# Kernel optimization log

Measured on AMD Instinct MI355X. Metric: run time of the kernel, lower is better.

## Reference

```python
import jax, jax.numpy as jnp
import numpy as np

N = 100000      # n_entities + n_users (graph nodes)
E = 1600000     # edges
R = 8           # relations
D = 64          # entity_dim
DR = 64         # relation_dim
EPS = 1e-12


def setup_inputs() -> dict:
    key = jax.random.key(0)
    ks = jax.random.split(key, 16)
    inp = {
        'entity_emb': jax.random.normal(ks[0], (N, D), jnp.float32) * 0.1,
        'rel_emb':    jax.random.normal(ks[1], (R, DR), jnp.float32) * 0.1,
        'W_R':        jax.random.normal(ks[2], (R, D, DR), jnp.float32) * 0.1,
        'W1_0': jax.random.normal(ks[3], (32, 64), jnp.float32) * 0.1,
        'b1_0': jax.random.normal(ks[4], (32,), jnp.float32) * 0.1,
        'W2_0': jax.random.normal(ks[5], (32, 64), jnp.float32) * 0.1,
        'b2_0': jax.random.normal(ks[6], (32,), jnp.float32) * 0.1,
        'W1_1': jax.random.normal(ks[7], (16, 32), jnp.float32) * 0.1,
        'b1_1': jax.random.normal(ks[8], (16,), jnp.float32) * 0.1,
        'W2_1': jax.random.normal(ks[9], (16, 32), jnp.float32) * 0.1,
        'b2_1': jax.random.normal(ks[10], (16,), jnp.float32) * 0.1,
        'src':   jax.random.randint(ks[11], (E,), 0, N, dtype=jnp.int32),
        'dst':   jax.random.randint(ks[12], (E,), 0, N, dtype=jnp.int32),
        'etype': jax.random.randint(ks[13], (E,), 0, R, dtype=jnp.int32),
    }
    return inp


def _l2_normalize(x):
    # F.normalize(x, p=2, dim=1)
    n = jnp.linalg.norm(x, axis=1, keepdims=True)
    return x / jnp.maximum(n, EPS)


def reference(entity_emb, rel_emb, W_R, W1_0, b1_0, W2_0, b2_0,
              W1_1, b1_1, W2_1, b2_1, src, dst, etype):
    # ---- compute_attention: per-edge relation-specific projection ----
    # proj[n, r, :] = entity_emb[n] @ W_R[r]   -> [N, R, DR]
    proj = jnp.einsum('nd,rdk->nrk', entity_emb, W_R)
    r_mul_t = proj[src, etype]          # [E, DR] (edges.src)
    r_mul_h = proj[dst, etype]          # [E, DR] (edges.dst)
    r_e = rel_emb[etype]                # [E, DR]
    att = jnp.sum(r_mul_t * jnp.tanh(r_mul_h + r_e), axis=-1)  # [E]

    # ---- edge_softmax: normalize over incoming edges of each dst ----
    m = jax.ops.segment_max(att, dst, num_segments=N)           # [N]
    ex = jnp.exp(att - m[dst])
    s = jax.ops.segment_sum(ex, dst, num_segments=N)            # [N]
    a = ex / s[dst]                                             # [E]

    # ---- bi-interaction aggregator layers ----
    def agg_layer(x, W1, b1, W2, b2):
        msg = x[src] * a[:, None]                               # u_mul_e
        Nh = jax.ops.segment_sum(msg, dst, num_segments=N)      # sum to dst
        out1 = jax.nn.leaky_relu(jnp.matmul(x + Nh, W1.T) + b1, 0.01)
        out2 = jax.nn.leaky_relu(jnp.matmul(x * Nh, W2.T) + b2, 0.01)
        return _l2_normalize(out1 + out2)

    ego = entity_emb
    h1 = agg_layer(ego, W1_0, b1_0, W2_0, b2_0)   # [N, 32]
    h2 = agg_layer(h1, W1_1, b1_1, W2_1, b2_1)    # [N, 16]
    all_embed = jnp.concatenate([ego, h1, h2], axis=1)  # [N, 112]
    return all_embed
```

## Files before the change

kernel.cpp:

```cpp
#include <hip/hip_runtime.h>
#include <hip/hip_bf16.h>
#include <math.h>

#define NN 100000
#define NE 1600000
#define NR 8
#define DD 64
#define DDR 64

typedef __attribute__((ext_vector_type(8))) short bf8v;
typedef __attribute__((ext_vector_type(4))) float f4v;

__device__ __forceinline__ unsigned enc_f(float f) {
    unsigned u = __float_as_uint(f);
    return (u & 0x80000000u) ? ~u : (u | 0x80000000u);
}
__device__ __forceinline__ float dec_f(unsigned u) {
    return (u & 0x80000000u) ? __uint_as_float(u & 0x7FFFFFFFu) : __uint_as_float(~u);
}

__device__ __forceinline__ float bflo(unsigned u) { return __uint_as_float(u << 16); }
__device__ __forceinline__ float bfhi(unsigned u) { return __uint_as_float(u & 0xFFFF0000u); }
__device__ __forceinline__ short f2bfs(float x) {
    __hip_bfloat16 h = __float2bfloat16(x);
    return *reinterpret_cast<short*>(&h);
}

__device__ __forceinline__ float tanh_fast(float x) {
    x = fminf(fmaxf(x, -15.f), 15.f);
    float e = __expf(2.f * x);
    return (e - 1.f) * __builtin_amdgcn_rcpf(e + 1.f);
}

__global__ void __launch_bounds__(256)
k_projm(const float* __restrict__ emb, const float* __restrict__ WR,
        unsigned short* __restrict__ proj)
{
    int t = threadIdx.x;
    int wv = t >> 6, l = t & 63;
    int lo = l & 15, hi = l >> 4;
    int r = blockIdx.y;
    int colbase = (wv & 1) * 32;
    int nwbase = blockIdx.x * 128 + (wv >> 1) * 64;

    const float* __restrict__ wb = WR + (long)r * (DD * DDR) + (hi * 8) * DDR + colbase + lo;
    bf8v B00, B01, B10, B11;
#pragma unroll
    for (int j = 0; j < 8; ++j) {
        B00[j] = f2bfs(wb[(0 * 32 + j) * DDR + 0]);
        B01[j] = f2bfs(wb[(1 * 32 + j) * DDR + 0]);
        B10[j] = f2bfs(wb[(0 * 32 + j) * DDR + 16]);
        B11[j] = f2bfs(wb[(1 * 32 + j) * DDR + 16]);
    }

    for (int nt = 0; nt < 4; ++nt) {
        int nb = nwbase + nt * 16;
        int arow = nb + lo;
        float4 xa0 = make_float4(0.f, 0.f, 0.f, 0.f), xa1 = xa0, xb0 = xa0, xb1 = xa0;
        if (arow < NN) {
            const float* __restrict__ xr = emb + (long)arow * DD + hi * 8;
            xa0 = *(const float4*)(xr);
            xa1 = *(const float4*)(xr + 4);
            xb0 = *(const float4*)(xr + 32);
            xb1 = *(const float4*)(xr + 36);
        }
        bf8v A0, A1;
        A0[0] = f2bfs(xa0.x); A0[1] = f2bfs(xa0.y); A0[2] = f2bfs(xa0.z); A0[3] = f2bfs(xa0.w);
        A0[4] = f2bfs(xa1.x); A0[5] = f2bfs(xa1.y); A0[6] = f2bfs(xa1.z); A0[7] = f2bfs(xa1.w);
        A1[0] = f2bfs(xb0.x); A1[1] = f2bfs(xb0.y); A1[2] = f2bfs(xb0.z); A1[3] = f2bfs(xb0.w);
        A1[4] = f2bfs(xb1.x); A1[5] = f2bfs(xb1.y); A1[6] = f2bfs(xb1.z); A1[7] = f2bfs(xb1.w);

        f4v acc0 = {0.f, 0.f, 0.f, 0.f}, acc1 = {0.f, 0.f, 0.f, 0.f};
        acc0 = __builtin_amdgcn_mfma_f32_16x16x32_bf16(A0, B00, acc0, 0, 0, 0);
        acc0 = __builtin_amdgcn_mfma_f32_16x16x32_bf16(A1, B01, acc0, 0, 0, 0);
        acc1 = __builtin_amdgcn_mfma_f32_16x16x32_bf16(A0, B10, acc1, 0, 0, 0);
        acc1 = __builtin_amdgcn_mfma_f32_16x16x32_bf16(A1, B11, acc1, 0, 0, 0);

#pragma unroll
        for (int i = 0; i < 4; ++i) {
            int rr = nb + hi * 4 + i;
            if (rr < NN) {
                long obase = ((long)r * NN + rr) * DDR + colbase + lo;
                proj[obase]      = (unsigned short)f2bfs(acc0[i]);
                proj[obase + 16] = (unsigned short)f2bfs(acc1[i]);
            }
        }
    }
}

__global__ void k_hist(const int* __restrict__ dst, unsigned* __restrict__ cnt)
{
    int e = blockIdx.x * blockDim.x + threadIdx.x;
    if (e >= NE) return;
    atomicAdd(cnt + dst[e], 1u);
}

__global__ void k_base(const unsigned* __restrict__ cnt, unsigned* __restrict__ gcur,
                       unsigned* __restrict__ base, unsigned* __restrict__ curs)
{
    int i = blockIdx.x * blockDim.x + threadIdx.x;
    int lane = threadIdx.x & 63;
    unsigned v = (i < NN) ? cnt[i] : 0u;
    unsigned p = v;
#pragma unroll
    for (int off = 1; off < 64; off <<= 1) {
        unsigned q = __shfl_up(p, off);
        if (lane >= off) p += q;
    }
    unsigned tot = __shfl(p, 63);
    unsigned gb = 0;
    if (lane == 0) gb = atomicAdd(gcur, tot);
    gb = __shfl(gb, 0);
    if (i < NN) {
        unsigned b = gb + p - v;
        base[i] = b;
        curs[i] = b;
    }
}

__global__ void k_scatter2(const int* __restrict__ dst, const int* __restrict__ src,
                           const int* __restrict__ et, unsigned* __restrict__ curs,
                           unsigned* __restrict__ srcet)
{
    int e = blockIdx.x * blockDim.x + threadIdx.x;
    if (e >= NE) return;
    unsigned pos = atomicAdd(curs + dst[e], 1u);
    srcet[pos] = (unsigned)src[e] | ((unsigned)et[e] << 28);
}

__global__ void __launch_bounds__(256)
k_mega0(const float* __restrict__ emb, const unsigned* __restrict__ proj,
        const float* __restrict__ rel,
        const unsigned* __restrict__ cnt, const unsigned* __restrict__ basep,
        const unsigned* __restrict__ srcet, float* __restrict__ acsr,
        const float* __restrict__ W1, const float* __restrict__ b1,
        const float* __restrict__ W2, const float* __restrict__ b2,
        float* __restrict__ out)
{
    __shared__ float W1T[64][33];
    __shared__ float W2T[64][33];
    __shared__ float sm1[4][64];
    __shared__ float sm2[4][64];
    __shared__ float att_s[4][64];
    int t = threadIdx.x;
#pragma unroll
    for (int i = 0; i < 8; ++i) {
        int idx = i * 256 + t;
        W1T[idx & 63][idx >> 6] = W1[idx];
        W2T[idx & 63][idx >> 6] = W2[idx];
    }
    int wv = t >> 6, lane = t & 63;
    int g = blockIdx.x * 4 + wv;
    int deg = (int)cnt[g];
    long b = basep[g];
    float Nh = 0.f;
    if (deg > 0 && deg <= 64) {
        unsigned se = 0;
        if (lane < deg) se = srcet[b + lane];
        int gi = lane >> 4;
        int lj = lane & 15;
        for (int k0 = 0; k0 < deg; k0 += 4) {
            int ei = k0 + gi;
            unsigned sei = __shfl(se, ei);
            int s = (int)(sei & 0x0FFFFFFFu);
            int r = (int)(sei >> 28);
            uint2 tv = *(const uint2*)(proj + ((long)r * NN + s) * 32 + lj * 2);
            uint2 hv = *(const uint2*)(proj + ((long)r * NN + g) * 32 + lj * 2);
            float4 rv = *(const float4*)(rel + r * DDR + lj * 4);
            float sum = bflo(tv.x) * tanh_fast(bflo(hv.x) + rv.x)
                      + bfhi(tv.x) * tanh_fast(bfhi(hv.x) + rv.y)
                      + bflo(tv.y) * tanh_fast(bflo(hv.y) + rv.z)
                      + bfhi(tv.y) * tanh_fast(bfhi(hv.y) + rv.w);
#pragma unroll
            for (int off = 8; off; off >>= 1) sum += __shfl_xor(sum, off);
            if (lj == 0 && ei < deg) att_s[wv][ei] = sum;
        }
        float attv = (lane < deg) ? att_s[wv][lane] : -3.4e38f;
        float m = attv;
#pragma unroll
        for (int off = 32; off; off >>= 1) m = fmaxf(m, __shfl_xor(m, off));
        float exv = (lane < deg) ? __expf(attv - m) : 0.f;
        float s_ = exv;
#pragma unroll
        for (int off = 32; off; off >>= 1) s_ += __shfl_xor(s_, off);
        float inv = 1.f / s_;
        if (lane < deg) acsr[b + lane] = exv * inv;
        float acc = 0.f;
        int i = 0;
        for (; i + 1 < deg; i += 2) {
            float a0 = __shfl(exv, i), a1 = __shfl(exv, i + 1);
            int s0 = (int)(__shfl(se, i) & 0x0FFFFFFFu);
            int s1 = (int)(__shfl(se, i + 1) & 0x0FFFFFFFu);
            float v0 = emb[(long)s0 * DD + lane];
            float v1 = emb[(long)s1 * DD + lane];
            acc = fmaf(v0, a0, acc);
            acc = fmaf(v1, a1, acc);
        }
        if (i < deg) {
            float a0 = __shfl(exv, i);
            int s0 = (int)(__shfl(se, i) & 0x0FFFFFFFu);
            acc = fmaf(emb[(long)s0 * DD + lane], a0, acc);
        }
        Nh = acc * inv;
    } else if (deg > 64) {
        float m = -3.4e38f;
        for (int i = 0; i < deg; ++i) {
            unsigned sei = srcet[b + i];
            int s = (int)(sei & 0x0FFFFFFFu);
            int r = (int)(sei >> 28);
            float pv = __uint_as_float(((unsigned)((const unsigned short*)proj)[((long)r * NN + s) * DDR + lane]) << 16);
            float dv = __uint_as_float(((unsigned)((const unsigned short*)proj)[((long)r * NN + g) * DDR + lane]) << 16);
            float rv = rel[r * DDR + lane];
            float term = pv * tanh_fast(dv + rv);
#pragma unroll
            for (int off = 32; off; off >>= 1) term += __shfl_xor(term, off);
            if (lane == 0) acsr[b + i] = term;
            m = fmaxf(m, term);
        }
        float s_ = 0.f;
        for (int i = lane; i < deg; i += 64) s_ += __expf(acsr[b + i] - m);
#pragma unroll
        for (int off = 32; off; off >>= 1) s_ += __shfl_xor(s_, off);
        float inv = 1.f / s_;
        float acc = 0.f;
        for (int i = 0; i < deg; ++i) {
            float raw = acsr[b + i];
            float a = __expf(raw - m) * inv;
            int s = (int)(srcet[b + i] & 0x0FFFFFFFu);
            acc = fmaf(emb[(long)s * DD + lane], a, acc);
            if (lane == 0) acsr[b + i] = a;
        }
        Nh = acc;
    }
    float x = emb[(long)g * DD + lane];
    sm1[wv][lane] = x + Nh;
    sm2[wv][lane] = x * Nh;
    __syncthreads();
    int j = lane & 31;
    const float* __restrict__ WT = (lane < 32) ? &W1T[0][0] : &W2T[0][0];
    const float* __restrict__ sm = (lane < 32) ? &sm1[wv][0] : &sm2[wv][0];
    float accm = (lane < 32) ? b1[j] : b2[j];
#pragma unroll 8
    for (int dd = 0; dd < 64; ++dd)
        accm = fmaf(sm[dd], WT[dd * 33 + j], accm);
    accm = (accm >= 0.f) ? accm : 0.01f * accm;
    float other = __shfl_down(accm, 32);
    float h = accm + other;
    float ss = h * h;
#pragma unroll
    for (int off = 16; off; off >>= 1) ss += __shfl_xor(ss, off);
    float hn = h / fmaxf(sqrtf(ss), 1e-12f);
    out[(long)g * 112 + lane] = x;
    if (lane < 32) out[(long)g * 112 + 64 + j] = hn;
}

__global__ void __launch_bounds__(256)
k_mega1(const float* __restrict__ acsr, const unsigned* __restrict__ srcet,
        const unsigned* __restrict__ cnt, const unsigned* __restrict__ basep,
        const float* __restrict__ W1, const float* __restrict__ b1,
        const float* __restrict__ W2, const float* __restrict__ b2,
        float* __restrict__ out)
{
    __shared__ float W1T[32][17];
    __shared__ float W2T[32][17];
    __shared__ float sm1[8][32];
    __shared__ float sm2[8][32];
    int t = threadIdx.x;
#pragma unroll
    for (int i = 0; i < 2; ++i) {
        int idx = i * 256 + t;
        W1T[idx & 31][idx >> 5] = W1[idx];
        W2T[idx & 31][idx >> 5] = W2[idx];
    }
    int grp = t >> 5, l5 = t & 31;
    int g = blockIdx.x * 8 + grp;
    int deg = (int)cnt[g];
    float acc = 0.f;
    if (deg > 0) {
        long b = basep[g];
        unsigned se = 0; float a = 0.f;
        if (l5 < deg) { se = srcet[b + l5]; a = acsr[b + l5]; }
        int dmin = (deg < 32) ? deg : 32;
        int i = 0;
        for (; i + 1 < dmin; i += 2) {
            float a0 = __shfl(a, i, 32), a1 = __shfl(a, i + 1, 32);
            int s0 = (int)(__shfl(se, i, 32) & 0x0FFFFFFFu);
            int s1 = (int)(__shfl(se, i + 1, 32) & 0x0FFFFFFFu);
            float v0 = out[(long)s0 * 112 + 64 + l5];
            float v1 = out[(long)s1 * 112 + 64 + l5];
            acc = fmaf(v0, a0, acc);
            acc = fmaf(v1, a1, acc);
        }
        if (i < dmin) {
            float a0 = __shfl(a, i, 32);
            int s0 = (int)(__shfl(se, i, 32) & 0x0FFFFFFFu);
            acc = fmaf(out[(long)s0 * 112 + 64 + l5], a0, acc);
        }
        for (int k = 32; k < deg; ++k) {
            float ak = acsr[b + k];
            int sk = (int)(srcet[b + k] & 0x0FFFFFFFu);
            acc = fmaf(out[(long)sk * 112 + 64 + l5], ak, acc);
        }
    }
    float x = out[(long)g * 112 + 64 + l5];
    sm1[grp][l5] = x + acc;
    sm2[grp][l5] = x * acc;
    __syncthreads();
    int j = l5 & 15;
    const float* __restrict__ WT = (l5 < 16) ? &W1T[0][0] : &W2T[0][0];
    const float* __restrict__ sm = (l5 < 16) ? &sm1[grp][0] : &sm2[grp][0];
    float accm = (l5 < 16) ? b1[j] : b2[j];
#pragma unroll 8
    for (int dd = 0; dd < 32; ++dd)
        accm = fmaf(sm[dd], WT[dd * 17 + j], accm);
    accm = (accm >= 0.f) ? accm : 0.01f * accm;
    float other = __shfl_down(accm, 16, 32);
    float h = accm + other;
    float ss = h * h;
#pragma unroll
    for (int off = 8; off; off >>= 1) ss += __shfl_xor(ss, off);
    float hn = h / fmaxf(sqrtf(ss), 1e-12f);
    if (l5 < 16) out[(long)g * 112 + 96 + j] = hn;
}

__global__ void k_att(const float* __restrict__ emb, const float* __restrict__ rel,
                      const float* __restrict__ WR, const int* __restrict__ src,
                      const int* __restrict__ dst, const int* __restrict__ et,
                      float* __restrict__ att, unsigned* __restrict__ mkey)
{
    int e = (int)((blockIdx.x * blockDim.x + threadIdx.x) >> 6);
    int lane = threadIdx.x & 63;
    if (e >= NE) return;
    int s = src[e], d = dst[e], r = et[e];
    const float* __restrict__ es = emb + (long)s * DD;
    const float* __restrict__ eh = emb + (long)d * DD;
    const float* __restrict__ w  = WR + r * (DD * DDR) + lane;
    float at = 0.f, ah = 0.f;
#pragma unroll 8
    for (int dd = 0; dd < DD; ++dd) {
        float ws = w[dd * DDR];
        at = fmaf(es[dd], ws, at);
        ah = fmaf(eh[dd], ws, ah);
    }
    float term = at * tanhf(ah + rel[r * DDR + lane]);
#pragma unroll
    for (int off = 32; off; off >>= 1) term += __shfl_xor(term, off);
    if (lane == 0) {
        att[e] = term;
        atomicMax(mkey + d, enc_f(term));
    }
}

__global__ void k_expsum(const int* __restrict__ dst, float* __restrict__ att,
                         const unsigned* __restrict__ mkey, float* __restrict__ ssum)
{
    int e = blockIdx.x * blockDim.x + threadIdx.x;
    if (e >= NE) return;
    int d = dst[e];
    float ex = expf(att[e] - dec_f(mkey[d]));
    att[e] = ex;
    atomicAdd(ssum + d, ex);
}

__global__ void k_agg0(const float* __restrict__ emb, const int* __restrict__ src,
                       const int* __restrict__ dst, float* __restrict__ att,
                       const float* __restrict__ ssum, float* __restrict__ Nh)
{
    int e = (int)((blockIdx.x * blockDim.x + threadIdx.x) >> 6);
    int lane = threadIdx.x & 63;
    if (e >= NE) return;
    int s = src[e], d = dst[e];
    float a = att[e] / ssum[d];
    if (lane == 0) att[e] = a;
    float v = emb[(long)s * DD + lane] * a;
    atomicAdd(Nh + (long)d * DD + lane, v);
}

__global__ void k_agg1(const float* __restrict__ out, const int* __restrict__ src,
                       const int* __restrict__ dst, const float* __restrict__ att,
                       float* __restrict__ Nh1)
{
    int idx = blockIdx.x * blockDim.x + threadIdx.x;
    int e = idx >> 5;
    int j = idx & 31;
    if (e >= NE) return;
    int s = src[e], d = dst[e];
    float a = att[e];
    float v = out[(long)s * 112 + 64 + j] * a;
    atomicAdd(Nh1 + (long)d * 32 + j, v);
}

#define NPB0 32
__global__ void __launch_bounds__(256)
k_node0t(const float* __restrict__ emb, const float* __restrict__ Nh,
         const float* __restrict__ W1, const float* __restrict__ b1,
         const float* __restrict__ W2, const float* __restrict__ b2,
         float* __restrict__ out)
{
    __shared__ float W1T[64][33];
    __shared__ float W2T[64][33];
    int t = threadIdx.x;
#pragma unroll
    for (int i = 0; i < 8; ++i) {
        int idx = i * 256 + t;
        W1T[idx & 63][idx >> 6] = W1[idx];
        W2T[idx & 63][idx >> 6] = W2[idx];
    }
    __syncthreads();
    int wv = t >> 6, lane = t & 63, j = lane & 31;
    const float* __restrict__ WT = (lane < 32) ? &W1T[0][0] : &W2T[0][0];
    float bj = (lane < 32) ? b1[j] : b2[j];
    int n0 = blockIdx.x * NPB0;
    int n1 = (n0 + NPB0 < NN) ? n0 + NPB0 : NN;
    for (int node = n0 + wv; node < n1; node += 4) {
        const float* __restrict__ x  = emb + (long)node * DD;
        const float* __restrict__ nh = Nh + (long)node * DD;
        float acc = 0.f;
#pragma unroll 8
        for (int dd = 0; dd < DD; ++dd) {
            float xv = x[dd], nv = nh[dd];
            float v = (lane < 32) ? (xv + nv) : (xv * nv);
            acc = fmaf(v, WT[dd * 33 + j], acc);
        }
        acc += bj;
        acc = (acc >= 0.f) ? acc : 0.01f * acc;
        float other = __shfl_down(acc, 32);
        float h = acc + other;
        float ss = h * h;
#pragma unroll
        for (int off = 16; off; off >>= 1) ss += __shfl_xor(ss, off);
        float hn = h / fmaxf(sqrtf(ss), 1e-12f);
        out[(long)node * 112 + lane] = x[lane];
        if (lane < 32) out[(long)node * 112 + 64 + j] = hn;
    }
}

#define NPB1 32
__global__ void __launch_bounds__(256)
k_node1t(const float* __restrict__ outbuf, const float* __restrict__ Nh1,
         const float* __restrict__ W1, const float* __restrict__ b1,
         const float* __restrict__ W2, const float* __restrict__ b2,
         float* __restrict__ out)
{
    __shared__ float W1T[32][17];
    __shared__ float W2T[32][17];
    int t = threadIdx.x;
#pragma unroll
    for (int i = 0; i < 2; ++i) {
        int idx = i * 256 + t;
        W1T[idx & 31][idx >> 5] = W1[idx];
        W2T[idx & 31][idx >> 5] = W2[idx];
    }
    __syncthreads();
    int grp = t >> 5;
    int l5 = t & 31, j = l5 & 15;
    const float* __restrict__ WT = (l5 < 16) ? &W1T[0][0] : &W2T[0][0];
    float bj = (l5 < 16) ? b1[j] : b2[j];
    int n0 = blockIdx.x * NPB1;
    int n1 = (n0 + NPB1 < NN) ? n0 + NPB1 : NN;
    for (int node = n0 + grp; node < n1; node += 8) {
        const float* __restrict__ x  = outbuf + (long)node * 112 + 64;
        const float* __restrict__ nh = Nh1 + (long)node * 32;
        float acc = 0.f;
#pragma unroll 8
        for (int dd = 0; dd < 32; ++dd) {
            float xv = x[dd], nv = nh[dd];
            float v = (l5 < 16) ? (xv + nv) : (xv * nv);
            acc = fmaf(v, WT[dd * 17 + j], acc);
        }
        acc += bj;
        acc = (acc >= 0.f) ? acc : 0.01f * acc;
        float other = __shfl_down(acc, 16, 32);
        float h = acc + other;
        float ss = h * h;
#pragma unroll
        for (int off = 8; off; off >>= 1) ss += __shfl_xor(ss, off);
        float hn = h / fmaxf(sqrtf(ss), 1e-12f);
        if (l5 < 16) out[(long)node * 112 + 96 + j] = hn;
    }
}

extern "C" void kernel_launch(void* const* d_in, const int* in_sizes, int n_in,
                              void* d_out, int out_size, void* d_ws, size_t ws_size,
                              hipStream_t stream) {
    const float* emb  = (const float*)d_in[0];
    const float* rel  = (const float*)d_in[1];
    const float* WR   = (const float*)d_in[2];
    const float* W1_0 = (const float*)d_in[3];
    const float* b1_0 = (const float*)d_in[4];
    const float* W2_0 = (const float*)d_in[5];
    const float* b2_0 = (const float*)d_in[6];
    const float* W1_1 = (const float*)d_in[7];
    const float* b1_1 = (const float*)d_in[8];
    const float* W2_1 = (const float*)d_in[9];
    const float* b2_1 = (const float*)d_in[10];
    const int*   src  = (const int*)d_in[11];
    const int*   dst  = (const int*)d_in[12];
    const int*   et   = (const int*)d_in[13];
    float* out = (float*)d_out;

    unsigned* cnt   = (unsigned*)d_ws;
    unsigned* gcur  = cnt + NN;
    unsigned* basep = cnt + NN + 64;
    unsigned* curs  = cnt + 2 * NN + 64;
    float* acsr  = (float*)d_ws + 3 * NN + 64;
    unsigned* srcet = (unsigned*)(acsr + NE);
    unsigned* proj = srcet + NE;

    size_t need = ((size_t)3 * NN + 64 + 2 * (size_t)NE) * 4
                + (size_t)NN * NR * DDR * 2;

    if (ws_size >= need) {
        hipMemsetAsync(d_ws, 0, (size_t)(NN + 64) * sizeof(unsigned), stream);
        k_hist<<<dim3((NE + 255) / 256), dim3(256), 0, stream>>>(dst, cnt);
        k_projm<<<dim3((NN + 127) / 128, NR), dim3(256), 0, stream>>>(
            emb, WR, (unsigned short*)proj);
        k_base<<<dim3((NN + 255) / 256), dim3(256), 0, stream>>>(cnt, gcur, basep, curs);
        k_scatter2<<<dim3((NE + 255) / 256), dim3(256), 0, stream>>>(
            dst, src, et, curs, srcet);
        k_mega0<<<dim3((NN + 3) / 4), dim3(256), 0, stream>>>(
            emb, proj, rel, cnt, basep, srcet, acsr,
            W1_0, b1_0, W2_0, b2_0, out);
        k_mega1<<<dim3((NN + 7) / 8), dim3(256), 0, stream>>>(
            acsr, srcet, cnt, basep, W1_1, b1_1, W2_1, b2_1, out);
    } else {
        unsigned* mkey = (unsigned*)d_ws;
        float* ssum = (float*)d_ws + NN;
        float* fNh0 = (float*)d_ws + 2 * NN;
        float* fNh1 = (float*)d_ws + (2 + DD) * NN;
        float* fatt = (float*)d_ws + (2 + DD + 32) * NN;
        hipMemsetAsync(d_ws, 0, (size_t)(2 + DD + 32) * NN * sizeof(float), stream);
        k_att<<<dim3((int)(((long)NE * 64 + 255) / 256)), dim3(256), 0, stream>>>(
            emb, rel, WR, src, dst, et, fatt, mkey);
        k_expsum<<<dim3((NE + 255) / 256), dim3(256), 0, stream>>>(dst, fatt, mkey, ssum);
        k_agg0<<<dim3((int)(((long)NE * 64 + 255) / 256)), dim3(256), 0, stream>>>(
            emb, src, dst, fatt, ssum, fNh0);
        k_node0t<<<dim3((NN + NPB0 - 1) / NPB0), dim3(256), 0, stream>>>(
            emb, fNh0, W1_0, b1_0, W2_0, b2_0, out);
        k_agg1<<<dim3((int)(((long)NE * 32 + 255) / 256)), dim3(256), 0, stream>>>(
            out, src, dst, fatt, fNh1);
        k_node1t<<<dim3((NN + NPB1 - 1) / NPB1), dim3(256), 0, stream>>>(
            out, fNh1, W1_1, b1_1, W2_1, b2_1, out);
    }
}
```

Baseline: 491.5 us.

## Fold attention into per-node W_R-projected tanh vectors and bf16 gather copies

Rewrites the attention score algebraically: att = (x_src W_r)·tanh(x_dst W_r + rel_r) = x_src · (W_r tanh(...)). A new MFMA kernel precomputes for each destination node and relation the 64-vector W_r·tanh(proj+rel). The edge loop then needs only a gather of the source embedding, which is also the aggregation operand, so score and weighted sum happen in one pass. That pass uses a one-pass softmax without max subtraction and clamps the exponent at 60. It also adds bf16 copies of the embeddings and of h1 to halve gather bytes, at the cost of a second projection pass over an extra 100 MB buffer and reduced precision.

```diff
diff --git a/kernel.cpp b/kernel.cpp
--- a/kernel.cpp
+++ b/kernel.cpp
@@ -18,14 +18,14 @@
 __device__ __forceinline__ float dec_f(unsigned u) {
     return (u & 0x80000000u) ? __uint_as_float(u & 0x7FFFFFFFu) : __uint_as_float(~u);
 }
-
-__device__ __forceinline__ float bflo(unsigned u) { return __uint_as_float(u << 16); }
-__device__ __forceinline__ float bfhi(unsigned u) { return __uint_as_float(u & 0xFFFF0000u); }
+__device__ __forceinline__ float bfs2f(unsigned short u) { return __uint_as_float(((unsigned)u) << 16); }
 __device__ __forceinline__ short f2bfs(float x) {
     __hip_bfloat16 h = __float2bfloat16(x);
     return *reinterpret_cast<short*>(&h);
 }
-
+__device__ __forceinline__ unsigned pack2bf(short a, short b) {
+    return (unsigned)(unsigned short)a | ((unsigned)(unsigned short)b << 16);
+}
 __device__ __forceinline__ float tanh_fast(float x) {
     x = fminf(fmaxf(x, -15.f), 15.f);
     float e = __expf(2.f * x);
@@ -34,7 +34,8 @@
 
 __global__ void __launch_bounds__(256)
 k_projm(const float* __restrict__ emb, const float* __restrict__ WR,
-        unsigned short* __restrict__ proj)
+        const float* __restrict__ rel,
+        unsigned short* __restrict__ tproj, unsigned* __restrict__ embh)
 {
     int t = threadIdx.x;
     int wv = t >> 6, l = t & 63;
@@ -52,6 +53,8 @@
         B10[j] = f2bfs(wb[(0 * 32 + j) * DDR + 16]);
         B11[j] = f2bfs(wb[(1 * 32 + j) * DDR + 16]);
     }
+    float rv0 = rel[r * DDR + colbase + lo];
+    float rv1 = rel[r * DDR + colbase + lo + 16];
 
     for (int nt = 0; nt < 4; ++nt) {
         int nb = nwbase + nt * 16;
@@ -70,6 +73,14 @@
         A1[0] = f2bfs(xb0.x); A1[1] = f2bfs(xb0.y); A1[2] = f2bfs(xb0.z); A1[3] = f2bfs(xb0.w);
         A1[4] = f2bfs(xb1.x); A1[5] = f2bfs(xb1.y); A1[6] = f2bfs(xb1.z); A1[7] = f2bfs(xb1.w);
 
+        if (r == 0 && arow < NN) {
+            unsigned* er = embh + (long)arow * 32 + hi * 4;
+            er[0]  = pack2bf(A0[0], A0[1]); er[1]  = pack2bf(A0[2], A0[3]);
+            er[2]  = pack2bf(A0[4], A0[5]); er[3]  = pack2bf(A0[6], A0[7]);
+            er[16] = pack2bf(A1[0], A1[1]); er[17] = pack2bf(A1[2], A1[3]);
+            er[18] = pack2bf(A1[4], A1[5]); er[19] = pack2bf(A1[6], A1[7]);
+        }
+
         f4v acc0 = {0.f, 0.f, 0.f, 0.f}, acc1 = {0.f, 0.f, 0.f, 0.f};
         acc0 = __builtin_amdgcn_mfma_f32_16x16x32_bf16(A0, B00, acc0, 0, 0, 0);
         acc0 = __builtin_amdgcn_mfma_f32_16x16x32_bf16(A1, B01, acc0, 0, 0, 0);
@@ -81,8 +92,58 @@
             int rr = nb + hi * 4 + i;
             if (rr < NN) {
                 long obase = ((long)r * NN + rr) * DDR + colbase + lo;
-                proj[obase]      = (unsigned short)f2bfs(acc0[i]);
-                proj[obase + 16] = (unsigned short)f2bfs(acc1[i]);
+                tproj[obase]      = (unsigned short)f2bfs(tanh_fast(acc0[i] + rv0));
+                tproj[obase + 16] = (unsigned short)f2bfs(tanh_fast(acc1[i] + rv1));
+            }
+        }
+    }
+}
+
+__global__ void __launch_bounds__(256)
+k_projw2(const unsigned short* __restrict__ tproj, const float* __restrict__ WR,
+         unsigned short* __restrict__ w2h)
+{
+    int t = threadIdx.x;
+    int wv = t >> 6, l = t & 63;
+    int lo = l & 15, hi = l >> 4;
+    int r = blockIdx.y;
+    int colbase = (wv & 1) * 32;
+    int nwbase = blockIdx.x * 128 + (wv >> 1) * 64;
+
+    const float* __restrict__ wb0 = WR + (long)r * (DD * DDR) + (long)(colbase + lo) * DDR + hi * 8;
+    const float* __restrict__ wb1 = wb0 + 16 * DDR;
+    bf8v B00, B01, B10, B11;
+#pragma unroll
+    for (int j = 0; j < 8; ++j) {
+        B00[j] = f2bfs(wb0[j]);
+        B01[j] = f2bfs(wb0[32 + j]);
+        B10[j] = f2bfs(wb1[j]);
+        B11[j] = f2bfs(wb1[32 + j]);
+    }
+
+    for (int nt = 0; nt < 4; ++nt) {
+        int nb = nwbase + nt * 16;
+        int arow = nb + lo;
+        bf8v A0, A1;
+#pragma unroll
+        for (int j = 0; j < 8; ++j) { A0[j] = 0; A1[j] = 0; }
+        if (arow < NN) {
+            const unsigned short* ar = tproj + ((long)r * NN + arow) * DDR + hi * 8;
+            A0 = *(const bf8v*)(ar);
+            A1 = *(const bf8v*)(ar + 32);
+        }
+        f4v acc0 = {0.f, 0.f, 0.f, 0.f}, acc1 = {0.f, 0.f, 0.f, 0.f};
+        acc0 = __builtin_amdgcn_mfma_f32_16x16x32_bf16(A0, B00, acc0, 0, 0, 0);
+        acc0 = __builtin_amdgcn_mfma_f32_16x16x32_bf16(A1, B01, acc0, 0, 0, 0);
+        acc1 = __builtin_amdgcn_mfma_f32_16x16x32_bf16(A0, B10, acc1, 0, 0, 0);
+        acc1 = __builtin_amdgcn_mfma_f32_16x16x32_bf16(A1, B11, acc1, 0, 0, 0);
+#pragma unroll
+        for (int i = 0; i < 4; ++i) {
+            int rr = nb + hi * 4 + i;
+            if (rr < NN) {
+                long obase = ((long)r * NN + rr) * DDR + colbase + lo;
+                w2h[obase]      = (unsigned short)f2bfs(acc0[i]);
+                w2h[obase + 16] = (unsigned short)f2bfs(acc1[i]);
             }
         }
     }
@@ -129,19 +190,19 @@
 }
 
 __global__ void __launch_bounds__(256)
-k_mega0(const float* __restrict__ emb, const unsigned* __restrict__ proj,
-        const float* __restrict__ rel,
-        const unsigned* __restrict__ cnt, const unsigned* __restrict__ basep,
-        const unsigned* __restrict__ srcet, float* __restrict__ acsr,
-        const float* __restrict__ W1, const float* __restrict__ b1,
-        const float* __restrict__ W2, const float* __restrict__ b2,
-        float* __restrict__ out)
+k_mega0w(const float* __restrict__ emb, const unsigned short* __restrict__ embh,
+         const unsigned short* __restrict__ w2h,
+         const unsigned* __restrict__ cnt, const unsigned* __restrict__ basep,
+         const unsigned* __restrict__ srcet, float* __restrict__ acsr,
+         unsigned short* __restrict__ h1h,
+         const float* __restrict__ W1, const float* __restrict__ b1,
+         const float* __restrict__ W2, const float* __restrict__ b2,
+         float* __restrict__ out)
 {
     __shared__ float W1T[64][33];
     __shared__ float W2T[64][33];
     __shared__ float sm1[4][64];
     __shared__ float sm2[4][64];
-    __shared__ float att_s[4][64];
     int t = threadIdx.x;
 #pragma unroll
     for (int i = 0; i < 8; ++i) {
@@ -155,82 +216,64 @@
     long b = basep[g];
     float Nh = 0.f;
     if (deg > 0 && deg <= 64) {
+        float w0 = bfs2f(w2h[((long)0 * NN + g) * DDR + lane]);
+        float w1_ = bfs2f(w2h[((long)1 * NN + g) * DDR + lane]);
+        float w2_ = bfs2f(w2h[((long)2 * NN + g) * DDR + lane]);
+        float w3 = bfs2f(w2h[((long)3 * NN + g) * DDR + lane]);
+        float w4 = bfs2f(w2h[((long)4 * NN + g) * DDR + lane]);
+        float w5 = bfs2f(w2h[((long)5 * NN + g) * DDR + lane]);
+        float w6 = bfs2f(w2h[((long)6 * NN + g) * DDR + lane]);
+        float w7 = bfs2f(w2h[((long)7 * NN + g) * DDR + lane]);
         unsigned se = 0;
         if (lane < deg) se = srcet[b + lane];
-        int gi = lane >> 4;
-        int lj = lane & 15;
-        for (int k0 = 0; k0 < deg; k0 += 4) {
-            int ei = k0 + gi;
-            unsigned sei = __shfl(se, ei);
-            int s = (int)(sei & 0x0FFFFFFFu);
-            int r = (int)(sei >> 28);
-            uint2 tv = *(const uint2*)(proj + ((long)r * NN + s) * 32 + lj * 2);
-            uint2 hv = *(const uint2*)(proj + ((long)r * NN + g) * 32 + lj * 2);
-            float4 rv = *(const float4*)(rel + r * DDR + lj * 4);
-            float sum = bflo(tv.x) * tanh_fast(bflo(hv.x) + rv.x)
-                      + bfhi(tv.x) * tanh_fast(bfhi(hv.x) + rv.y)
-                      + bflo(tv.y) * tanh_fast(bflo(hv.y) + rv.z)
-                      + bfhi(tv.y) * tanh_fast(bfhi(hv.y) + rv.w);
-#pragma unroll
-            for (int off = 8; off; off >>= 1) sum += __shfl_xor(sum, off);
-            if (lj == 0 && ei < deg) att_s[wv][ei] = sum;
-        }
-        float attv = (lane < deg) ? att_s[wv][lane] : -3.4e38f;
-        float m = attv;
-#pragma unroll
-        for (int off = 32; off; off >>= 1) m = fmaxf(m, __shfl_xor(m, off));
-        float exv = (lane < deg) ? __expf(attv - m) : 0.f;
-        float s_ = exv;
-#pragma unroll
-        for (int off = 32; off; off >>= 1) s_ += __shfl_xor(s_, off);
+        float acc = 0.f, s_ = 0.f, myexp = 0.f;
+        for (int i = 0; i < deg; i += 2) {
+            int i1 = (i + 1 < deg) ? i + 1 : i;
+            unsigned se0 = __shfl(se, i);
+            unsigned se1 = __shfl(se, i1);
+            int s0 = (int)(se0 & 0x0FFFFFFFu), r0 = (int)(se0 >> 28);
+            int s1 = (int)(se1 & 0x0FFFFFFFu), r1 = (int)(se1 >> 28);
+            float v0 = bfs2f(embh[(long)s0 * DD + lane]);
+            float v1 = bfs2f(embh[(long)s1 * DD + lane]);
+            float wa = (r0 & 4) ? ((r0 & 2) ? ((r0 & 1) ? w7 : w6) : ((r0 & 1) ? w5 : w4))
+                                : ((r0 & 2) ? ((r0 & 1) ? w3 : w2_) : ((r0 & 1) ? w1_ : w0));
+            float wbx = (r1 & 4) ? ((r1 & 2) ? ((r1 & 1) ? w7 : w6) : ((r1 & 1) ? w5 : w4))
+                                 : ((r1 & 2) ? ((r1 & 1) ? w3 : w2_) : ((r1 & 1) ? w1_ : w0));
+            float p0 = v0 * wa;
+            float p1 = v1 * wbx;
+#pragma unroll
+            for (int off = 32; off; off >>= 1) {
+                p0 += __shfl_xor(p0, off);
+                p1 += __shfl_xor(p1, off);
+            }
+            float ex0 = __expf(fminf(p0, 60.f));
+            float ex1 = (i + 1 < deg) ? __expf(fminf(p1, 60.f)) : 0.f;
+            if (lane == i) myexp = ex0;
+            if (lane == i + 1 && i + 1 < deg) myexp = ex1;
+            s_ += ex0 + ex1;
+            acc = fmaf(v0, ex0, fmaf(v1, ex1, acc));
+        }
         float inv = 1.f / s_;
-        if (lane < deg) acsr[b + lane] = exv * inv;
-        float acc = 0.f;
-        int i = 0;
-        for (; i + 1 < deg; i += 2) {
-            float a0 = __shfl(exv, i), a1 = __shfl(exv, i + 1);
-            int s0 = (int)(__shfl(se, i) & 0x0FFFFFFFu);
-            int s1 = (int)(__shfl(se, i + 1) & 0x0FFFFFFFu);
-            float v0 = emb[(long)s0 * DD + lane];
-            float v1 = emb[(long)s1 * DD + lane];
-            acc = fmaf(v0, a0, acc);
-            acc = fmaf(v1, a1, acc);
-        }
-        if (i < deg) {
-            float a0 = __shfl(exv, i);
-            int s0 = (int)(__shfl(se, i) & 0x0FFFFFFFu);
-            acc = fmaf(emb[(long)s0 * DD + lane], a0, acc);
-        }
+        if (lane < deg) acsr[b + lane] = myexp * inv;
         Nh = acc * inv;
     } else if (deg > 64) {
-        float m = -3.4e38f;
+        float s_ = 0.f, acc = 0.f;
         for (int i = 0; i < deg; ++i) {
             unsigned sei = srcet[b + i];
-            int s = (int)(sei & 0x0FFFFFFFu);
-            int r = (int)(sei >> 28);
-            float pv = __uint_as_float(((unsigned)((const unsigned short*)proj)[((long)r * NN + s) * DDR + lane]) << 16);
-            float dv = __uint_as_float(((unsigned)((const unsigned short*)proj)[((long)r * NN + g) * DDR + lane]) << 16);
-            float rv = rel[r * DDR + lane];
-            float term = pv * tanh_fast(dv + rv);
-#pragma unroll
-            for (int off = 32; off; off >>= 1) term += __shfl_xor(term, off);
-            if (lane == 0) acsr[b + i] = term;
-            m = fmaxf(m, term);
-        }
-        float s_ = 0.f;
-        for (int i = lane; i < deg; i += 64) s_ += __expf(acsr[b + i] - m);
-#pragma unroll
-        for (int off = 32; off; off >>= 1) s_ += __shfl_xor(s_, off);
+            int s = (int)(sei & 0x0FFFFFFFu), r = (int)(sei >> 28);
+            float v = bfs2f(embh[(long)s * DD + lane]);
+            float wvl = bfs2f(w2h[((long)r * NN + g) * DDR + lane]);
+            float p = v * wvl;
+#pragma unroll
+            for (int off = 32; off; off >>= 1) p += __shfl_xor(p, off);
+            float ex = __expf(fminf(p, 60.f));
+            s_ += ex;
+            acc = fmaf(v, ex, acc);
+            if (lane == 0) acsr[b + i] = ex;
+        }
         float inv = 1.f / s_;
-        float acc = 0.f;
-        for (int i = 0; i < deg; ++i) {
-            float raw = acsr[b + i];
-            float a = __expf(raw - m) * inv;
-            int s = (int)(srcet[b + i] & 0x0FFFFFFFu);
-            acc = fmaf(emb[(long)s * DD + lane], a, acc);
-            if (lane == 0) acsr[b + i] = a;
-        }
-        Nh = acc;
+        for (int i = lane; i < deg; i += 64) acsr[b + i] *= inv;
+        Nh = acc * inv;
     }
     float x = emb[(long)g * DD + lane];
     sm1[wv][lane] = x + Nh;
@@ -251,12 +294,16 @@
     for (int off = 16; off; off >>= 1) ss += __shfl_xor(ss, off);
     float hn = h / fmaxf(sqrtf(ss), 1e-12f);
     out[(long)g * 112 + lane] = x;
-    if (lane < 32) out[(long)g * 112 + 64 + j] = hn;
+    if (lane < 32) {
+        out[(long)g * 112 + 64 + j] = hn;
+        h1h[(long)g * 32 + j] = (unsigned short)f2bfs(hn);
+    }
 }
 
 __global__ void __launch_bounds__(256)
 k_mega1(const float* __restrict__ acsr, const unsigned* __restrict__ srcet,
         const unsigned* __restrict__ cnt, const unsigned* __restrict__ basep,
+        const unsigned short* __restrict__ h1h,
         const float* __restrict__ W1, const float* __restrict__ b1,
         const float* __restrict__ W2, const float* __restrict__ b2,
         float* __restrict__ out)
@@ -286,20 +333,20 @@
             float a0 = __shfl(a, i, 32), a1 = __shfl(a, i + 1, 32);
             int s0 = (int)(__shfl(se, i, 32) & 0x0FFFFFFFu);
             int s1 = (int)(__shfl(se, i + 1, 32) & 0x0FFFFFFFu);
-            float v0 = out[(long)s0 * 112 + 64 + l5];
-            float v1 = out[(long)s1 * 112 + 64 + l5];
+            float v0 = bfs2f(h1h[(long)s0 * 32 + l5]);
+            float v1 = bfs2f(h1h[(long)s1 * 32 + l5]);
             acc = fmaf(v0, a0, acc);
             acc = fmaf(v1, a1, acc);
         }
         if (i < dmin) {
             float a0 = __shfl(a, i, 32);
             int s0 = (int)(__shfl(se, i, 32) & 0x0FFFFFFFu);
-            acc = fmaf(out[(long)s0 * 112 + 64 + l5], a0, acc);
+            acc = fmaf(bfs2f(h1h[(long)s0 * 32 + l5]), a0, acc);
         }
         for (int k = 32; k < deg; ++k) {
             float ak = acsr[b + k];
             int sk = (int)(srcet[b + k] & 0x0FFFFFFFu);
-            acc = fmaf(out[(long)sk * 112 + 64 + l5], ak, acc);
+            acc = fmaf(bfs2f(h1h[(long)sk * 32 + l5]), ak, acc);
         }
     }
     float x = out[(long)g * 112 + 64 + l5];
@@ -505,24 +552,30 @@
     unsigned* curs  = cnt + 2 * NN + 64;
     float* acsr  = (float*)d_ws + 3 * NN + 64;
     unsigned* srcet = (unsigned*)(acsr + NE);
-    unsigned* proj = srcet + NE;
+    unsigned short* tproj = (unsigned short*)(srcet + NE);
+    unsigned short* w2h = tproj + (size_t)NR * NN * DDR;
+    unsigned* embh = (unsigned*)(w2h + (size_t)NR * NN * DDR);
+    unsigned short* h1h = (unsigned short*)(embh + (size_t)NN * 32);
 
     size_t need = ((size_t)3 * NN + 64 + 2 * (size_t)NE) * 4
-                + (size_t)NN * NR * DDR * 2;
+                + 2 * (size_t)NR * NN * DDR * 2
+                + (size_t)NN * 32 * 4 + (size_t)NN * 16 * 4;
 
     if (ws_size >= need) {
         hipMemsetAsync(d_ws, 0, (size_t)(NN + 64) * sizeof(unsigned), stream);
         k_hist<<<dim3((NE + 255) / 256), dim3(256), 0, stream>>>(dst, cnt);
         k_projm<<<dim3((NN + 127) / 128, NR), dim3(256), 0, stream>>>(
-            emb, WR, (unsigned short*)proj);
+            emb, WR, rel, tproj, embh);
+        k_projw2<<<dim3((NN + 127) / 128, NR), dim3(256), 0, stream>>>(
+            tproj, WR, w2h);
         k_base<<<dim3((NN + 255) / 256), dim3(256), 0, stream>>>(cnt, gcur, basep, curs);
         k_scatter2<<<dim3((NE + 255) / 256), dim3(256), 0, stream>>>(
             dst, src, et, curs, srcet);
-        k_mega0<<<dim3((NN + 3) / 4), dim3(256), 0, stream>>>(
-            emb, proj, rel, cnt, basep, srcet, acsr,
+        k_mega0w<<<dim3((NN + 3) / 4), dim3(256), 0, stream>>>(
+            emb, (const unsigned short*)embh, w2h, cnt, basep, srcet, acsr, h1h,
             W1_0, b1_0, W2_0, b2_0, out);
         k_mega1<<<dim3((NN + 7) / 8), dim3(256), 0, stream>>>(
-            acsr, srcet, cnt, basep, W1_1, b1_1, W2_1, b2_1, out);
+            acsr, srcet, cnt, basep, h1h, W1_1, b1_1, W2_1, b2_1, out);
     } else {
         unsigned* mkey = (unsigned*)d_ws;
         float* ssum = (float*)d_ws + NN;
```

After: 544.3 us. 10.8% more time.
